# Kernel optimization log

Hardware: AMD Instinct MI355X
Metric: run time of the kernel (lower is better)

Reference implementation:

```python
import jax, jax.numpy as jnp
import numpy as np

# LLaMA-style decoder config (shrunken for reference): L layers, hidden D, H heads,
# SwiGLU width F, vocab V, LoRA rank R.
B, S, D, H, F, V, L, R = 2, 512, 1024, 16, 4096, 32000, 2, 16
DH = D // H
LORA_ALPHA = 32.0
EPS = 1e-5
ROPE_THETA = 10000.0


def setup_inputs() -> dict:
    key = jax.random.key(0)
    ks = iter(jax.random.split(key, 40))
    def n(shape, std=0.02):
        return jax.random.normal(next(ks), shape, jnp.float32) * std
    return {
        "input_ids": jax.random.randint(next(ks), (B, S), 0, V),
        "attention_mask": jnp.ones((B, S), jnp.int32),
        "embed": n((V, D)),
        "ln1": jnp.ones((L, D), jnp.float32),
        "ln2": jnp.ones((L, D), jnp.float32),
        "wq": n((L, D, D)), "aq": n((L, D, R)), "bq": n((L, R, D), 0.01),
        "wk": n((L, D, D)), "ak": n((L, D, R)), "bk": n((L, R, D), 0.01),
        "wv": n((L, D, D)), "av": n((L, D, R)), "bv": n((L, R, D), 0.01),
        "wo": n((L, D, D)), "ao": n((L, D, R)), "bo": n((L, R, D), 0.01),
        "wg": n((L, D, F)), "ag": n((L, D, R)), "bg": n((L, R, F), 0.01),
        "wu": n((L, D, F)), "au": n((L, D, R)), "bu": n((L, R, F), 0.01),
        "wd": n((L, F, D)), "ad": n((L, F, R)), "bd": n((L, R, D), 0.01),
        "final_ln": jnp.ones((D,), jnp.float32),
        "lm_head_w": n((D, V)),
        "value_w": n((D, 1)),
        "value_b": jnp.zeros((1,), jnp.float32),
    }


def _rmsnorm(x, w):
    return x * jax.lax.rsqrt(jnp.mean(x * x, axis=-1, keepdims=True) + EPS) * w


def _lin_lora(x, w, a, b):
    # base matmul + low-rank LoRA update scaled by alpha/r (dropout=eval/off)
    return x @ w + ((x @ a) @ b) * (LORA_ALPHA / R)


def _rope_cache(seq_len):
    half = DH // 2
    inv = 1.0 / (ROPE_THETA ** (jnp.arange(half, dtype=jnp.float32) / half))
    ang = jnp.arange(seq_len, dtype=jnp.float32)[:, None] * inv  # [S, half]
    ang = jnp.concatenate([ang, ang], axis=-1)                   # [S, DH]
    return jnp.cos(ang), jnp.sin(ang)


def _apply_rope(x, cos, sin):  # x: [B,S,H,DH]
    h = DH // 2
    rot = jnp.concatenate([-x[..., h:], x[..., :h]], axis=-1)
    return x * cos[None, :, None, :] + rot * sin[None, :, None, :]


def reference(input_ids, attention_mask, embed, ln1, ln2,
              wq, aq, bq, wk, ak, bk, wv, av, bv, wo, ao, bo,
              wg, ag, bg, wu, au, bu, wd, ad, bd,
              final_ln, lm_head_w, value_w, value_b):
    h = embed[input_ids]  # [B,S,D]
    cos, sin = _rope_cache(S)
    causal = jnp.tril(jnp.ones((S, S), bool))
    keep = causal[None, None, :, :] & (attention_mask[:, None, None, :] > 0)
    bias = jnp.where(keep, 0.0, -1e9)  # [B,1,S,S]
    scale = 1.0 / jnp.sqrt(jnp.float32(DH))

    for i in range(L):
        # --- self-attention block ---
        x = _rmsnorm(h, ln1[i])
        q = _lin_lora(x, wq[i], aq[i], bq[i]).reshape(B, S, H, DH)
        k = _lin_lora(x, wk[i], ak[i], bk[i]).reshape(B, S, H, DH)
        v = _lin_lora(x, wv[i], av[i], bv[i]).reshape(B, S, H, DH)
        q = _apply_rope(q, cos, sin)
        k = _apply_rope(k, cos, sin)
        scores = jnp.einsum("bqhd,bkhd->bhqk", q, k) * scale + bias
        attn = jax.nn.softmax(scores, axis=-1)
        o = jnp.einsum("bhqk,bkhd->bqhd", attn, v).reshape(B, S, D)
        h = h + _lin_lora(o, wo[i], ao[i], bo[i])
        # --- SwiGLU MLP block ---
        x = _rmsnorm(h, ln2[i])
        g = jax.nn.silu(_lin_lora(x, wg[i], ag[i], bg[i]))
        u = _lin_lora(x, wu[i], au[i], bu[i])
        h = h + _lin_lora(g * u, wd[i], ad[i], bd[i])

    h = _rmsnorm(h, final_ln)          # HF hidden_states[-1] is post final norm
    logits = h @ lm_head_w             # [B,S,V]
    values = (h @ value_w)[..., 0] + value_b[0]  # [B,S] (squeeze(-1))
    return logits, values
```

## Files before the change

### kernel.cpp

```cpp
#include <hip/hip_runtime.h>
#include <math.h>

constexpr int B = 2, S = 512, D = 1024, H = 16, F = 4096, V = 32000, L = 2, R = 16, DH = 64;
constexpr int BS = B * S;
constexpr float LORA_SCALE = 2.0f;
constexpr float EPS = 1e-5f;
constexpr int RS_QKV = 3 * D;
constexpr int RS_GU  = 2 * F;

typedef __attribute__((ext_vector_type(8))) __bf16 bf16x8;
typedef __attribute__((ext_vector_type(4))) float f32x4;

__device__ __forceinline__ unsigned short f2bf(float f) {
  unsigned u = __builtin_bit_cast(unsigned, f);
  unsigned r = (u + 0x7FFFu + ((u >> 16) & 1u)) >> 16;
  return (unsigned short)r;
}
__device__ __forceinline__ float bf2f(unsigned short us) {
  return __builtin_bit_cast(float, (unsigned)us << 16);
}
__device__ __forceinline__ void load_lds16(const void* g, void* l) {
  __builtin_amdgcn_global_load_lds((const __attribute__((address_space(1))) void*)g,
                                   (__attribute__((address_space(3))) void*)l, 16, 0, 0);
}

struct Ptr3 { const float* p[3]; };

__global__ void rope_cache_kernel(float* __restrict__ cosb, float* __restrict__ sinb) {
  int s = blockIdx.x, j = threadIdx.x;
  float inv = __expf(-(float)j * (9.210340371976184f / 32.0f));
  float ang = (float)s * inv;
  float c = cosf(ang), sn = sinf(ang);
  cosb[s * DH + j] = c;  cosb[s * DH + j + 32] = c;
  sinb[s * DH + j] = sn; sinb[s * DH + j + 32] = sn;
}

__global__ void embed_kernel(const int* __restrict__ ids, const float* __restrict__ emb,
                             float* __restrict__ h) {
  int row = blockIdx.x, t = threadIdx.x;
  int id = ids[row];
  ((float4*)(h + (size_t)row * D))[t] = ((const float4*)(emb + (size_t)id * D))[t];
}

__global__ void rmsnorm_bf16_kernel(const float* __restrict__ x, const float* __restrict__ w,
                                    unsigned short* __restrict__ y) {
  int row = blockIdx.x, t = threadIdx.x;
  float4 xv = ((const float4*)(x + (size_t)row * D))[t];
  float ss = xv.x * xv.x + xv.y * xv.y + xv.z * xv.z + xv.w * xv.w;
  __shared__ float red[256];
  red[t] = ss; __syncthreads();
  for (int s2 = 128; s2; s2 >>= 1) { if (t < s2) red[t] += red[t + s2]; __syncthreads(); }
  float rinv = rsqrtf(red[0] * (1.0f / D) + EPS);
  float4 wv = ((const float4*)w)[t];
  ushort4 o;
  o.x = f2bf(xv.x * rinv * wv.x); o.y = f2bf(xv.y * rinv * wv.y);
  o.z = f2bf(xv.z * rinv * wv.z); o.w = f2bf(xv.w * rinv * wv.w);
  ((ushort4*)(y + (size_t)row * D))[t] = o;
}

template <int NA>
__global__ void rms_lora_kernel(const float* __restrict__ hp, const float* __restrict__ w,
                                Ptr3 ap, unsigned short* __restrict__ xbf,
                                unsigned short* __restrict__ t2e) {
  int row = blockIdx.x, t = threadIdx.x;
  int lane = t & 63;
  __shared__ float xs[D];
  __shared__ float red[256];
  float4 xv = ((const float4*)(hp + (size_t)row * D))[t];
  float ss = xv.x * xv.x + xv.y * xv.y + xv.z * xv.z + xv.w * xv.w;
  red[t] = ss; __syncthreads();
  for (int s2 = 128; s2; s2 >>= 1) { if (t < s2) red[t] += red[t + s2]; __syncthreads(); }
  float rinv = rsqrtf(red[0] * (1.0f / D) + EPS);
  float4 wv = ((const float4*)w)[t];
  float4 nx;
  nx.x = xv.x * rinv * wv.x; nx.y = xv.y * rinv * wv.y;
  nx.z = xv.z * rinv * wv.z; nx.w = xv.w * rinv * wv.w;
  xs[t * 4 + 0] = nx.x; xs[t * 4 + 1] = nx.y; xs[t * 4 + 2] = nx.z; xs[t * 4 + 3] = nx.w;
  ushort4 o;
  o.x = f2bf(nx.x); o.y = f2bf(nx.y); o.z = f2bf(nx.z); o.w = f2bf(nx.w);
  ((ushort4*)(xbf + (size_t)row * D))[t] = o;
  if (t >= NA * 16 && t < 64) t2e[(size_t)row * 64 + t] = 0;
  __syncthreads();
  int n = t & 15, g = t >> 4;
#pragma unroll
  for (int ad = 0; ad < NA; ++ad) {
    const float* a = ap.p[ad];
    float s = 0.0f;
    for (int k = g; k < D; k += 16) s = fmaf(xs[k], a[k * 16 + n], s);
    s += __shfl_xor(s, 16);
    s += __shfl_xor(s, 32);
    if (lane < 16) red[(t >> 6) * 16 + n] = s;
    __syncthreads();
    if (t < 16) t2e[(size_t)row * 64 + ad * 16 + t] =
        f2bf(LORA_SCALE * (red[t] + red[t + 16] + red[t + 32] + red[t + 48]));
    if (ad + 1 < NA) __syncthreads();
  }
}

__global__ void lora_o_kernel(const unsigned short* __restrict__ xb, const float* __restrict__ a,
                              unsigned short* __restrict__ t2e) {
  int row = blockIdx.x, t = threadIdx.x;
  int lane = t & 63;
  __shared__ float xs[D];
  __shared__ float red[64];
  for (int k = t; k < D; k += 256) xs[k] = bf2f(xb[(size_t)row * D + k]);
  if (t >= 16 && t < 64) t2e[(size_t)row * 64 + t] = 0;
  __syncthreads();
  int n = t & 15, g = t >> 4;
  float s = 0.0f;
  for (int k = g; k < D; k += 16) s = fmaf(xs[k], a[k * 16 + n], s);
  s += __shfl_xor(s, 16);
  s += __shfl_xor(s, 32);
  if (lane < 16) red[(t >> 6) * 16 + n] = s;
  __syncthreads();
  if (t < 16) t2e[(size_t)row * 64 + t] =
      f2bf(LORA_SCALE * (red[t] + red[t + 16] + red[t + 32] + red[t + 48]));
}

__global__ void silu_lora_kernel(const unsigned short* __restrict__ gub, const float* __restrict__ a,
                                 unsigned short* __restrict__ gbf, unsigned short* __restrict__ t2e) {
  int row = blockIdx.x, t = threadIdx.x;
  int lane = t & 63;
  __shared__ float xs[F];
  __shared__ float red[64];
#pragma unroll
  for (int i2 = 0; i2 < 2; ++i2) {
    int idx = i2 * 256 + t;
    uint4 gv = ((const uint4*)(gub + (size_t)row * RS_GU))[idx];
    uint4 uv = ((const uint4*)(gub + (size_t)row * RS_GU + F))[idx];
    const unsigned* gw = (const unsigned*)&gv;
    const unsigned* uw = (const unsigned*)&uv;
    unsigned short go[8];
#pragma unroll
    for (int q = 0; q < 4; ++q) {
      float g0 = bf2f((unsigned short)(gw[q] & 0xffff)), g1 = bf2f((unsigned short)(gw[q] >> 16));
      float u0 = bf2f((unsigned short)(uw[q] & 0xffff)), u1 = bf2f((unsigned short)(uw[q] >> 16));
      float r0 = g0 / (1.0f + __expf(-g0)) * u0;
      float r1 = g1 / (1.0f + __expf(-g1)) * u1;
      xs[idx * 8 + q * 2] = r0; xs[idx * 8 + q * 2 + 1] = r1;
      go[q * 2] = f2bf(r0); go[q * 2 + 1] = f2bf(r1);
    }
    *(uint4*)(gbf + (size_t)row * F + idx * 8) = *(const uint4*)go;
  }
  if (t >= 16 && t < 64) t2e[(size_t)row * 64 + t] = 0;
  __syncthreads();
  int n = t & 15, g = t >> 4;
  float s = 0.0f;
  for (int k = g; k < F; k += 16) s = fmaf(xs[k], a[k * 16 + n], s);
  s += __shfl_xor(s, 16);
  s += __shfl_xor(s, 32);
  if (lane < 16) red[(t >> 6) * 16 + n] = s;
  __syncthreads();
  if (t < 16) t2e[(size_t)row * 64 + t] =
      f2bf(LORA_SCALE * (red[t] + red[t + 16] + red[t + 32] + red[t + 48]));
}

struct BD { const float* p0; const float* p1; const float* p2;
            unsigned short* dst; int NA; int logW; int nelem; };
struct BDs { BD d[8]; };
__global__ void bext_many_kernel(BDs da) {
  int gid = blockIdx.x * 256 + threadIdx.x;
  int di = 0;
  while (gid >= da.d[di].nelem) { gid -= da.d[di].nelem; ++di; }
  const BD dd = da.d[di];
  int n = gid >> 6, kk = gid & 63;
  int W = 1 << dd.logW;
  int sel = n >> dd.logW;
  const float* bp = (sel == 0) ? dd.p0 : (sel == 1) ? dd.p1 : dd.p2;
  float v = 0.0f;
  if ((kk >> 4) == sel && sel < dd.NA)
    v = bp[(size_t)(kk & 15) * W + (n & (W - 1))];
  dd.dst[(size_t)n * 64 + kk] = f2bf(v);
}

struct TD { const float* src; unsigned short* dst; int K; int N; int nblk; };
struct TDs { TD d[15]; };
__global__ __launch_bounds__(256) void transpose_many_kernel(TDs da) {
  __shared__ unsigned short tile[64 * 136];
  int bid = blockIdx.x;
  int di = 0;
  while (bid >= da.d[di].nblk) { bid -= da.d[di].nblk; ++di; }
  const TD dd = da.d[di];
  int nbx = dd.N >> 6;
  int n0 = (bid % nbx) * 64, k0 = (bid / nbx) * 128;
  int t = threadIdx.x;
  int rr = t >> 4, c4 = (t & 15) << 2;
  float4 v[8];
#pragma unroll
  for (int i = 0; i < 8; ++i)
    v[i] = *(const float4*)(dd.src + (size_t)(k0 + i * 16 + rr) * dd.N + n0 + c4);
#pragma unroll
  for (int i = 0; i < 8; ++i) {
    int row = i * 16 + rr;
    tile[(c4 + 0) * 136 + (row ^ ((((c4 + 0) >> 2) & 7) << 2))] = f2bf(v[i].x);
    tile[(c4 + 1) * 136 + (row ^ ((((c4 + 1) >> 2) & 7) << 2))] = f2bf(v[i].y);
    tile[(c4 + 2) * 136 + (row ^ ((((c4 + 2) >> 2) & 7) << 2))] = f2bf(v[i].z);
    tile[(c4 + 3) * 136 + (row ^ ((((c4 + 3) >> 2) & 7) << 2))] = f2bf(v[i].w);
  }
  __syncthreads();
  ushort4 o[8];
#pragma unroll
  for (int i = 0; i < 8; ++i) {
    int flat = i * 256 + t;
    int n = flat >> 5, cw = flat & 31;
    int kb = (cw * 4) ^ (((n >> 2) & 7) << 2);
    o[i] = *(const ushort4*)(tile + n * 136 + kb);
  }
#pragma unroll
  for (int i = 0; i < 8; ++i) {
    int flat = i * 256 + t;
    int n = flat >> 5, cw = flat & 31;
    *(ushort4*)(dd.dst + (size_t)(n0 + n) * dd.K + k0 + cw * 4) = o[i];
  }
}

template <int BN, bool ACC, bool EXT, int OM>
__global__ __launch_bounds__(256) void gemm_bf16_kernel(
    const unsigned short* __restrict__ A, const unsigned short* __restrict__ Bt,
    void* __restrict__ Cp, int M, int N, int K,
    const unsigned short* __restrict__ Ae, const unsigned short* __restrict__ Be,
    const float* __restrict__ cosb, const float* __restrict__ sinb) {
  constexpr int WM = (BN == 128) ? 2 : 4;
  constexpr int RW = 128 / WM;
  constexpr int MI = RW / 16;
  constexpr int BCH = BN / 32;
  __shared__ __align__(16) unsigned short As[2][128 * 64];
  __shared__ __align__(16) unsigned short Bs[2][BN * 64];
  int t = threadIdx.x;
  int lane = t & 63, wave = t >> 6;
  int wr = (BN == 128) ? (wave >> 1) : wave;
  int wc = (BN == 128) ? (wave & 1) : 0;
  int MT = gridDim.y, NT = gridDim.x;
  int nwg = MT * NT;
  int orig = blockIdx.y * NT + blockIdx.x;
  int qq = nwg >> 3, rr8 = nwg & 7;
  int xcd = orig & 7, pos = orig >> 3;
  int wg = (xcd < rr8) ? (xcd * (qq + 1) + pos) : (rr8 * (qq + 1) + (xcd - rr8) * qq + pos);
  int m0 = (wg % MT) * 128, n0 = (wg / MT) * BN;
  int fr = lane & 15, fq = lane >> 4;
  int xorv = fr & 7;
  f32x4 acc[MI][4] = {};
  int kIters = K / 64;
  int nIters = EXT ? kIters + 1 : kIters;

  auto STAGE = [&](int it, int buf) {
    bool ext = EXT && (it == kIters);
    int k0 = it * 64;
#pragma unroll
    for (int c = 0; c < 4; ++c) {
      int i = c * 256 + t;
      int row = i >> 3, c8 = i & 7;
      int sc = (c8 ^ (row & 7)) * 8;
      const unsigned short* src = ext ? (Ae + (size_t)(m0 + row) * 64 + sc)
                                      : (A + (size_t)(m0 + row) * K + k0 + sc);
      load_lds16(src, &As[buf][i * 8]);
    }
#pragma unroll
    for (int c = 0; c < BCH; ++c) {
      int i = c * 256 + t;
      int row = i >> 3, c8 = i & 7;
      int sc = (c8 ^ (row & 7)) * 8;
      const unsigned short* src = ext ? (Be + (size_t)(n0 + row) * 64 + sc)
                                      : (Bt + (size_t)(n0 + row) * K + k0 + sc);
      load_lds16(src, &Bs[buf][i * 8]);
    }
  };

  STAGE(0, 0);
  if (nIters > 1) STAGE(1, 1);
  int cur = 0;
  for (int it = 0; it < nIters; ++it) {
    if (it + 1 < nIters) {
      if constexpr (BN == 128) asm volatile("s_waitcnt vmcnt(8)" ::: "memory");
      else                     asm volatile("s_waitcnt vmcnt(6)" ::: "memory");
    } else {
      asm volatile("s_waitcnt vmcnt(0)" ::: "memory");
    }
    __builtin_amdgcn_s_barrier();
#pragma unroll
    for (int kk = 0; kk < 2; ++kk) {
      bf16x8 af[MI], bfr[4];
#pragma unroll
      for (int mi = 0; mi < MI; ++mi)
        af[mi] = *(const bf16x8*)(&As[cur][(wr * RW + mi * 16 + fr) * 64 + (((kk * 4 + fq) ^ xorv) << 3)]);
#pragma unroll
      for (int ni = 0; ni < 4; ++ni)
        bfr[ni] = *(const bf16x8*)(&Bs[cur][(wc * 64 + ni * 16 + fr) * 64 + (((kk * 4 + fq) ^ xorv) << 3)]);
#pragma unroll
      for (int mi = 0; mi < MI; ++mi)
#pragma unroll
        for (int ni = 0; ni < 4; ++ni)
          acc[mi][ni] = __builtin_amdgcn_mfma_f32_16x16x32_bf16(af[mi], bfr[ni], acc[mi][ni], 0, 0, 0);
    }
    __builtin_amdgcn_s_barrier();
    if (it + 2 < nIters) STAGE(it + 2, cur);
    cur ^= 1;
  }
  if constexpr (OM == 0) {
    float* C = (float*)Cp;
#pragma unroll
    for (int mi = 0; mi < MI; ++mi)
#pragma unroll
      for (int ni = 0; ni < 4; ++ni)
#pragma unroll
        for (int j = 0; j < 4; ++j) {
          int r = m0 + wr * RW + mi * 16 + fq * 4 + j;
          int cl = n0 + wc * 64 + ni * 16 + fr;
          size_t idx = (size_t)r * N + cl;
          float v = acc[mi][ni][j];
          C[idx] = ACC ? C[idx] + v : v;
        }
  } else {
    unsigned short* Cb = (unsigned short*)Cp;
#pragma unroll
    for (int mi = 0; mi < MI; ++mi)
#pragma unroll
      for (int j = 0; j < 4; ++j) {
        int r = m0 + wr * RW + mi * 16 + fq * 4 + j;
        if constexpr (OM == 2) {
          int s = r & (S - 1);
#pragma unroll
          for (int ni = 0; ni < 2; ++ni) {
            int cl0 = n0 + wc * 64 + ni * 16 + fr;
            int cl1 = cl0 + 32;
            float x0 = acc[mi][ni][j], x1 = acc[mi][ni + 2][j];
            if (cl0 < 2 * D) {
              int dh = cl0 & 63;
              float cz = cosb[s * DH + dh], sz = sinb[s * DH + dh];
              float y0 = x0 * cz - x1 * sz;
              float y1 = x1 * cz + x0 * sz;
              x0 = y0; x1 = y1;
            }
            Cb[(size_t)r * N + cl0] = f2bf(x0);
            Cb[(size_t)r * N + cl1] = f2bf(x1);
          }
        } else {
#pragma unroll
          for (int ni = 0; ni < 4; ++ni) {
            int cl = n0 + wc * 64 + ni * 16 + fr;
            Cb[(size_t)r * N + cl] = f2bf(acc[mi][ni][j]);
          }
        }
      }
  }
}

__global__ __launch_bounds__(512) void gemm256_kernel(
    const unsigned short* __restrict__ A, const unsigned short* __restrict__ Bt,
    float* __restrict__ C, int M, int N, int K) {
  __shared__ __align__(16) unsigned short As[2][256 * 64];
  __shared__ __align__(16) unsigned short Bs[2][256 * 64];
  int t = threadIdx.x;
  int lane = t & 63, wave = t >> 6;
  int wr = wave >> 2, wc = wave & 3;
  int MT = gridDim.y, NT = gridDim.x;
  int nwg = MT * NT;
  int orig = blockIdx.y * NT + blockIdx.x;
  int qq = nwg >> 3, rr8 = nwg & 7;
  int xcd = orig & 7, pos = orig >> 3;
  int wg = (xcd < rr8) ? (xcd * (qq + 1) + pos) : (rr8 * (qq + 1) + (xcd - rr8) * qq + pos);
  int m0 = (wg % MT) * 256, n0 = (wg / MT) * 256;
  int fr = lane & 15, fq = lane >> 4;
  int xorv = fr & 7;
  f32x4 acc[8][4] = {};
  int kIters = K / 64;

  auto STAGE = [&](int it, int buf) {
    int k0 = it * 64;
#pragma unroll
    for (int c = 0; c < 4; ++c) {
      int i = c * 512 + t;
      int row = i >> 3, c8 = i & 7;
      int sc = (c8 ^ (row & 7)) * 8;
      load_lds16(A + (size_t)(m0 + row) * K + k0 + sc, &As[buf][i * 8]);
    }
#pragma unroll
    for (int c = 0; c < 4; ++c) {
      int i = c * 512 + t;
      int row = i >> 3, c8 = i & 7;
      int sc = (c8 ^ (row & 7)) * 8;
      load_lds16(Bt + (size_t)(n0 + row) * K + k0 + sc, &Bs[buf][i * 8]);
    }
  };

  STAGE(0, 0);
  if (kIters > 1) STAGE(1, 1);
  int cur = 0;
  for (int it = 0; it < kIters; ++it) {
    if (it + 1 < kIters) asm volatile("s_waitcnt vmcnt(8)" ::: "memory");
    else                 asm volatile("s_waitcnt vmcnt(0)" ::: "memory");
    __builtin_amdgcn_s_barrier();
#pragma unroll
    for (int kk = 0; kk < 2; ++kk) {
      bf16x8 af[8], bfr[4];
#pragma unroll
      for (int mi = 0; mi < 8; ++mi)
        af[mi] = *(const bf16x8*)(&As[cur][(wr * 128 + mi * 16 + fr) * 64 + (((kk * 4 + fq) ^ xorv) << 3)]);
#pragma unroll
      for (int ni = 0; ni < 4; ++ni)
        bfr[ni] = *(const bf16x8*)(&Bs[cur][(wc * 64 + ni * 16 + fr) * 64 + (((kk * 4 + fq) ^ xorv) << 3)]);
#pragma unroll
      for (int mi = 0; mi < 8; ++mi)
#pragma unroll
        for (int ni = 0; ni < 4; ++ni)
          acc[mi][ni] = __builtin_amdgcn_mfma_f32_16x16x32_bf16(af[mi], bfr[ni], acc[mi][ni], 0, 0, 0);
    }
    __builtin_amdgcn_s_barrier();
    if (it + 2 < kIters) STAGE(it + 2, cur);
    cur ^= 1;
  }
#pragma unroll
  for (int mi = 0; mi < 8; ++mi)
#pragma unroll
    for (int ni = 0; ni < 4; ++ni)
#pragma unroll
      for (int j = 0; j < 4; ++j) {
        int r = m0 + wr * 128 + mi * 16 + fq * 4 + j;
        int cl = n0 + wc * 64 + ni * 16 + fr;
        C[(size_t)r * N + cl] = acc[mi][ni][j];
      }
}

__global__ __launch_bounds__(256) void attn_mfma_kernel(
    const unsigned short* __restrict__ qkvb, const int* __restrict__ amask,
    unsigned short* __restrict__ o) {
  __shared__ unsigned short Qs[64 * 72];
  __shared__ unsigned short Ks[64 * 72];
  __shared__ unsigned short Vt[64 * 72];
  __shared__ unsigned short Ps[4][16 * 72];
  __shared__ float msk[64];
  int bid = blockIdx.x;
  int qt = bid & 7, hh = (bid >> 3) & (H - 1), b = bid >> 7;
  int t = threadIdx.x;
  int lane = t & 63, w = t >> 6;
  int fr = lane & 15, fq = lane >> 4;
  size_t rowbase = (size_t)b * S;
  int q0 = qt * 64;
  const float scale = 0.125f;
#pragma unroll
  for (int c = 0; c < 2; ++c) {
    int i = c * 256 + t;
    int row = i >> 3, ch = i & 7;
    *(uint4*)(Qs + row * 72 + ch * 8) =
        *(const uint4*)(qkvb + (rowbase + q0 + row) * RS_QKV + hh * DH + ch * 8);
  }
  f32x4 oacc[4] = {};
  float m_old[4] = {-1e30f, -1e30f, -1e30f, -1e30f};
  float l[4] = {};
  int qbase = q0 + w * 16;
  for (int kt = 0; kt <= qt; ++kt) {
    int kk0 = kt * 64;
#pragma unroll
    for (int c = 0; c < 2; ++c) {
      int i = c * 256 + t;
      int row = i >> 3, ch = i & 7;
      uint4 kv = *(const uint4*)(qkvb + (rowbase + kk0 + row) * RS_QKV + D + hh * DH + ch * 8);
      *(uint4*)(Ks + row * 72 + ch * 8) = kv;
    }
#pragma unroll
    for (int c = 0; c < 2; ++c) {
      int idx = c * 256 + t;
      int rp = idx >> 4, dg = idx & 15;
      const unsigned short* vsrc = qkvb + (rowbase + kk0 + rp * 2) * RS_QKV + 2 * D + hh * DH + dg * 4;
      uint2 lo = *(const uint2*)vsrc;
      uint2 hi = *(const uint2*)(vsrc + RS_QKV);
      const unsigned short* ls = (const unsigned short*)&lo;
      const unsigned short* hs = (const unsigned short*)&hi;
#pragma unroll
      for (int q = 0; q < 4; ++q) {
        unsigned pk = (unsigned)ls[q] | ((unsigned)hs[q] << 16);
        *(unsigned*)(Vt + (dg * 4 + q) * 72 + rp * 2) = pk;
      }
    }
    if (t < 64) msk[t] = (amask[b * S + kk0 + t] > 0) ? 0.0f : -1e9f;
    __syncthreads();
    bf16x8 aq[2];
    aq[0] = *(const bf16x8*)(Qs + (w * 16 + fr) * 72 + fq * 8);
    aq[1] = *(const bf16x8*)(Qs + (w * 16 + fr) * 72 + 32 + fq * 8);
    f32x4 sacc[4];
#pragma unroll
    for (int ct = 0; ct < 4; ++ct) {
      bf16x8 bk0 = *(const bf16x8*)(Ks + (ct * 16 + fr) * 72 + fq * 8);
      bf16x8 bk1 = *(const bf16x8*)(Ks + (ct * 16 + fr) * 72 + 32 + fq * 8);
      f32x4 z = {};
      z = __builtin_amdgcn_mfma_f32_16x16x32_bf16(aq[0], bk0, z, 0, 0, 0);
      sacc[ct] = __builtin_amdgcn_mfma_f32_16x16x32_bf16(aq[1], bk1, z, 0, 0, 0);
    }
    float sv[4][4];
#pragma unroll
    for (int ct = 0; ct < 4; ++ct) {
      int kg = kk0 + ct * 16 + fr;
      float mk = msk[ct * 16 + fr];
#pragma unroll
      for (int j = 0; j < 4; ++j) {
        int qg = qbase + fq * 4 + j;
        float s = sacc[ct][j] * scale + mk;
        sv[ct][j] = (kg > qg) ? -1e9f : s;
      }
    }
    float mnew[4], f[4], rsum[4];
#pragma unroll
    for (int j = 0; j < 4; ++j) {
      float mt = fmaxf(fmaxf(sv[0][j], sv[1][j]), fmaxf(sv[2][j], sv[3][j]));
      for (int off = 1; off < 16; off <<= 1) mt = fmaxf(mt, __shfl_xor(mt, off));
      mnew[j] = fmaxf(m_old[j], mt);
      f[j] = __expf(m_old[j] - mnew[j]);
      float rs = 0.0f;
#pragma unroll
      for (int ct = 0; ct < 4; ++ct) {
        float e = __expf(sv[ct][j] - mnew[j]);
        sv[ct][j] = e;
        rs += e;
      }
      for (int off = 1; off < 16; off <<= 1) rs += __shfl_xor(rs, off);
      rsum[j] = rs;
      l[j] = l[j] * f[j] + rsum[j];
      m_old[j] = mnew[j];
#pragma unroll
      for (int dt = 0; dt < 4; ++dt) oacc[dt][j] *= f[j];
    }
#pragma unroll
    for (int ct = 0; ct < 4; ++ct)
#pragma unroll
      for (int j = 0; j < 4; ++j)
        Ps[w][(fq * 4 + j) * 72 + ct * 16 + fr] = f2bf(sv[ct][j]);
    __syncthreads();
    bf16x8 pa[2];
    pa[0] = *(const bf16x8*)(&Ps[w][fr * 72 + fq * 8]);
    pa[1] = *(const bf16x8*)(&Ps[w][fr * 72 + 32 + fq * 8]);
#pragma unroll
    for (int dt = 0; dt < 4; ++dt) {
      bf16x8 vb0 = *(const bf16x8*)(Vt + (dt * 16 + fr) * 72 + fq * 8);
      bf16x8 vb1 = *(const bf16x8*)(Vt + (dt * 16 + fr) * 72 + 32 + fq * 8);
      oacc[dt] = __builtin_amdgcn_mfma_f32_16x16x32_bf16(pa[0], vb0, oacc[dt], 0, 0, 0);
      oacc[dt] = __builtin_amdgcn_mfma_f32_16x16x32_bf16(pa[1], vb1, oacc[dt], 0, 0, 0);
    }
    __syncthreads();
  }
#pragma unroll
  for (int j = 0; j < 4; ++j) {
    float rinv = 1.0f / l[j];
    int qrow = qbase + fq * 4 + j;
#pragma unroll
    for (int dt = 0; dt < 4; ++dt)
      o[(rowbase + qrow) * D + hh * DH + dt * 16 + fr] = f2bf(oacc[dt][j] * rinv);
  }
}

__global__ void value_kernel(const unsigned short* __restrict__ hf, const float* __restrict__ vw,
                             const float* __restrict__ vb, float* __restrict__ out) {
  int row = blockIdx.x, t = threadIdx.x;
  float acc = 0.0f;
  for (int d = t; d < D; d += 256) acc = fmaf(bf2f(hf[(size_t)row * D + d]), vw[d], acc);
  __shared__ float red[256];
  red[t] = acc; __syncthreads();
  for (int s2 = 128; s2; s2 >>= 1) { if (t < s2) red[t] += red[t + s2]; __syncthreads(); }
  if (t == 0) out[row] = red[0] + vb[0];
}

extern "C" void kernel_launch(void* const* d_in, const int* in_sizes, int n_in,
                              void* d_out, int out_size, void* d_ws, size_t ws_size,
                              hipStream_t stream) {
  const int*   ids     = (const int*)d_in[0];
  const int*   amask   = (const int*)d_in[1];
  const float* emb     = (const float*)d_in[2];
  const float* ln1     = (const float*)d_in[3];
  const float* ln2     = (const float*)d_in[4];
  const float* wq = (const float*)d_in[5],  *aq = (const float*)d_in[6],  *bq = (const float*)d_in[7];
  const float* wk = (const float*)d_in[8],  *ak = (const float*)d_in[9],  *bk = (const float*)d_in[10];
  const float* wv = (const float*)d_in[11], *av = (const float*)d_in[12], *bv = (const float*)d_in[13];
  const float* wo = (const float*)d_in[14], *ao = (const float*)d_in[15], *bo = (const float*)d_in[16];
  const float* wg = (const float*)d_in[17], *ag = (const float*)d_in[18], *bg = (const float*)d_in[19];
  const float* wu = (const float*)d_in[20], *au = (const float*)d_in[21], *bu = (const float*)d_in[22];
  const float* wd = (const float*)d_in[23], *ad = (const float*)d_in[24], *bd = (const float*)d_in[25];
  const float* final_ln  = (const float*)d_in[26];
  const float* lm_head_w = (const float*)d_in[27];
  const float* value_w   = (const float*)d_in[28];
  const float* value_b   = (const float*)d_in[29];

  float* out    = (float*)d_out;
  float* logits = out;
  float* values = out + (size_t)BS * V;

  float* Wf = (float*)d_ws;
  float* cosb = Wf; Wf += S * DH;
  float* sinb = Wf; Wf += S * DH;
  float* h    = Wf; Wf += (size_t)BS * D;
  unsigned short* Wb = (unsigned short*)Wf;
  unsigned short* x_bf  = Wb; Wb += (size_t)BS * D;
  unsigned short* t2e   = Wb; Wb += (size_t)BS * 64;
  unsigned short* qg    = Wb; Wb += (size_t)BS * F;
  unsigned short* gu_bf = Wb; Wb += (size_t)BS * RS_GU;
  unsigned short* wqkvT = Wb; Wb += (size_t)L * 3 * D * D;
  unsigned short* woT   = Wb; Wb += (size_t)L * D * D;
  unsigned short* wguT  = Wb; Wb += (size_t)L * 2 * D * F;
  unsigned short* wdT   = Wb; Wb += (size_t)L * F * D;
  unsigned short* lmT   = Wb; Wb += (size_t)D * V;
  unsigned short* beQKV = Wb; Wb += (size_t)L * 3 * D * 64;
  unsigned short* beO   = Wb; Wb += (size_t)L * D * 64;
  unsigned short* beGU  = Wb; Wb += (size_t)L * 2 * F * 64;
  unsigned short* beD   = Wb; Wb += (size_t)L * D * 64;
  unsigned short* qkv_bf = qg;
  unsigned short* gbf    = qg;
  unsigned short* obf    = gu_bf;

  TDs td; int tblocks = 0; int di = 0;
  auto addT = [&](const float* s, unsigned short* dp, int K_, int N_) {
    td.d[di] = {s, dp, K_, N_, (K_ / 128) * (N_ / 64)};
    tblocks += td.d[di].nblk; ++di;
  };
  for (int l = 0; l < L; ++l) {
    size_t DD = (size_t)D * D, DF = (size_t)D * F;
    addT(wq + l * DD, wqkvT + (size_t)l * 3 * DD, D, D);
    addT(wk + l * DD, wqkvT + (size_t)l * 3 * DD + DD, D, D);
    addT(wv + l * DD, wqkvT + (size_t)l * 3 * DD + 2 * DD, D, D);
    addT(wo + l * DD, woT + l * DD, D, D);
    addT(wg + l * DF, wguT + (size_t)l * 2 * DF, D, F);
    addT(wu + l * DF, wguT + (size_t)l * 2 * DF + DF, D, F);
    addT(wd + l * DF, wdT + l * DF, F, D);
  }
  addT(lm_head_w, lmT, D, V);
  transpose_many_kernel<<<dim3(tblocks), 256, 0, stream>>>(td);

  BDs bd2; int belems = 0; di = 0;
  auto addB = [&](const float* p0, const float* p1, const float* p2,
                  unsigned short* dst, int NA, int logW, int N_) {
    bd2.d[di] = {p0, p1, p2, dst, NA, logW, N_ * 64};
    belems += N_ * 64; ++di;
  };
  for (int l = 0; l < L; ++l) {
    size_t oRD = (size_t)l * R * D, oRF = (size_t)l * R * F;
    addB(bq + oRD, bk + oRD, bv + oRD, beQKV + (size_t)l * 3 * D * 64, 3, 10, 3 * D);
    addB(bo + oRD, nullptr, nullptr,   beO   + (size_t)l * D * 64,     1, 10, D);
    addB(bg + oRF, bu + oRF, nullptr,  beGU  + (size_t)l * 2 * F * 64, 2, 12, 2 * F);
    addB(bd + oRD, nullptr, nullptr,   beD   + (size_t)l * D * 64,     1, 10, D);
  }
  bext_many_kernel<<<dim3(belems / 256), 256, 0, stream>>>(bd2);

  rope_cache_kernel<<<dim3(S), dim3(32), 0, stream>>>(cosb, sinb);
  embed_kernel<<<dim3(BS), dim3(256), 0, stream>>>(ids, emb, h);

  for (int l = 0; l < L; ++l) {
    size_t DD = (size_t)D * D, DF = (size_t)D * F;
    size_t oDR = (size_t)l * D * R, oFR = (size_t)l * F * R;

    { Ptr3 ap = {{aq + oDR, ak + oDR, av + oDR}};
      rms_lora_kernel<3><<<dim3(BS), 256, 0, stream>>>(h, ln1 + (size_t)l * D, ap, x_bf, t2e); }
    gemm_bf16_kernel<128, false, true, 2><<<dim3(3 * D / 128, BS / 128), 256, 0, stream>>>(
        x_bf, wqkvT + (size_t)l * 3 * DD, qkv_bf, BS, 3 * D, D,
        t2e, beQKV + (size_t)l * 3 * D * 64, cosb, sinb);

    attn_mfma_kernel<<<dim3(B * H * (S / 64)), 256, 0, stream>>>(qkv_bf, amask, obf);

    lora_o_kernel<<<dim3(BS), 256, 0, stream>>>(obf, ao + oDR, t2e);
    gemm_bf16_kernel<64, true, true, 0><<<dim3(D / 64, BS / 128), 256, 0, stream>>>(
        obf, woT + l * DD, h, BS, D, D, t2e, beO + (size_t)l * D * 64, nullptr, nullptr);

    { Ptr3 ap = {{ag + oDR, au + oDR, nullptr}};
      rms_lora_kernel<2><<<dim3(BS), 256, 0, stream>>>(h, ln2 + (size_t)l * D, ap, x_bf, t2e); }
    gemm_bf16_kernel<128, false, true, 1><<<dim3(2 * F / 128, BS / 128), 256, 0, stream>>>(
        x_bf, wguT + (size_t)l * 2 * DF, gu_bf, BS, 2 * F, D,
        t2e, beGU + (size_t)l * 2 * F * 64, nullptr, nullptr);

    silu_lora_kernel<<<dim3(BS), 256, 0, stream>>>(gu_bf, ad + oFR, gbf, t2e);

    gemm_bf16_kernel<64, true, true, 0><<<dim3(D / 64, BS / 128), 256, 0, stream>>>(
        gbf, wdT + l * DF, h, BS, D, F, t2e, beD + (size_t)l * D * 64, nullptr, nullptr);
  }

  rmsnorm_bf16_kernel<<<dim3(BS), 256, 0, stream>>>(h, final_ln, x_bf);
  gemm256_kernel<<<dim3(V / 256, BS / 256), 512, 0, stream>>>(x_bf, lmT, logits, BS, V, D);
  value_kernel<<<dim3(BS), 256, 0, stream>>>(x_bf, value_w, value_b, values);
}
```

Measured before the change: 1.004 ms.

## Widen weight transpose tiles, fuse value head into final norm, raise MFMA priority

The weight transpose kernel now handles 256-row K tiles with a new XOR swizzle and writes 16-byte vectors, which halves the block count and widens the stores. The value-head dot product is folded into the final RMSNorm kernel and uses fp32 normalized values, which removes one launch and a re-read of the bf16 activations. The bf16 GEMM main loop raises wave priority around the MFMA section. Risks are higher register and LDS use in the transpose kernel and a slight numeric change in the value output.

```diff
diff --git a/kernel.cpp b/kernel.cpp
--- a/kernel.cpp
+++ b/kernel.cpp
@@ -42,8 +42,9 @@
   ((float4*)(h + (size_t)row * D))[t] = ((const float4*)(emb + (size_t)id * D))[t];
 }
 
-__global__ void rmsnorm_bf16_kernel(const float* __restrict__ x, const float* __restrict__ w,
-                                    unsigned short* __restrict__ y) {
+__global__ void rmsnorm_value_kernel(const float* __restrict__ x, const float* __restrict__ w,
+                                     const float* __restrict__ vw, const float* __restrict__ vb,
+                                     unsigned short* __restrict__ y, float* __restrict__ values) {
   int row = blockIdx.x, t = threadIdx.x;
   float4 xv = ((const float4*)(x + (size_t)row * D))[t];
   float ss = xv.x * xv.x + xv.y * xv.y + xv.z * xv.z + xv.w * xv.w;
@@ -52,10 +53,18 @@
   for (int s2 = 128; s2; s2 >>= 1) { if (t < s2) red[t] += red[t + s2]; __syncthreads(); }
   float rinv = rsqrtf(red[0] * (1.0f / D) + EPS);
   float4 wv = ((const float4*)w)[t];
+  float4 nx;
+  nx.x = xv.x * rinv * wv.x; nx.y = xv.y * rinv * wv.y;
+  nx.z = xv.z * rinv * wv.z; nx.w = xv.w * rinv * wv.w;
   ushort4 o;
-  o.x = f2bf(xv.x * rinv * wv.x); o.y = f2bf(xv.y * rinv * wv.y);
-  o.z = f2bf(xv.z * rinv * wv.z); o.w = f2bf(xv.w * rinv * wv.w);
+  o.x = f2bf(nx.x); o.y = f2bf(nx.y); o.z = f2bf(nx.z); o.w = f2bf(nx.w);
   ((ushort4*)(y + (size_t)row * D))[t] = o;
+  float4 vv = ((const float4*)vw)[t];
+  float vd = nx.x * vv.x + nx.y * vv.y + nx.z * vv.z + nx.w * vv.w;
+  __syncthreads();
+  red[t] = vd; __syncthreads();
+  for (int s2 = 128; s2; s2 >>= 1) { if (t < s2) red[t] += red[t + s2]; __syncthreads(); }
+  if (t == 0) values[row] = red[0] + vb[0];
 }
 
 template <int NA>
@@ -176,41 +185,37 @@
 struct TD { const float* src; unsigned short* dst; int K; int N; int nblk; };
 struct TDs { TD d[15]; };
 __global__ __launch_bounds__(256) void transpose_many_kernel(TDs da) {
-  __shared__ unsigned short tile[64 * 136];
+  __shared__ unsigned short tile[64 * 264];
   int bid = blockIdx.x;
   int di = 0;
   while (bid >= da.d[di].nblk) { bid -= da.d[di].nblk; ++di; }
   const TD dd = da.d[di];
   int nbx = dd.N >> 6;
-  int n0 = (bid % nbx) * 64, k0 = (bid / nbx) * 128;
+  int n0 = (bid % nbx) * 64, k0 = (bid / nbx) * 256;
   int t = threadIdx.x;
   int rr = t >> 4, c4 = (t & 15) << 2;
-  float4 v[8];
-#pragma unroll
-  for (int i = 0; i < 8; ++i)
+  float4 v[16];
+#pragma unroll
+  for (int i = 0; i < 16; ++i)
     v[i] = *(const float4*)(dd.src + (size_t)(k0 + i * 16 + rr) * dd.N + n0 + c4);
 #pragma unroll
-  for (int i = 0; i < 8; ++i) {
-    int row = i * 16 + rr;
-    tile[(c4 + 0) * 136 + (row ^ ((((c4 + 0) >> 2) & 7) << 2))] = f2bf(v[i].x);
-    tile[(c4 + 1) * 136 + (row ^ ((((c4 + 1) >> 2) & 7) << 2))] = f2bf(v[i].y);
-    tile[(c4 + 2) * 136 + (row ^ ((((c4 + 2) >> 2) & 7) << 2))] = f2bf(v[i].z);
-    tile[(c4 + 3) * 136 + (row ^ ((((c4 + 3) >> 2) & 7) << 2))] = f2bf(v[i].w);
+  for (int i = 0; i < 16; ++i) {
+    int k = i * 16 + rr;
+#pragma unroll
+    for (int j = 0; j < 4; ++j) {
+      int n = c4 + j;
+      float e = (j == 0) ? v[i].x : (j == 1) ? v[i].y : (j == 2) ? v[i].z : v[i].w;
+      tile[n * 264 + (k ^ ((n & 3) << 3))] = f2bf(e);
+    }
   }
   __syncthreads();
-  ushort4 o[8];
 #pragma unroll
   for (int i = 0; i < 8; ++i) {
     int flat = i * 256 + t;
     int n = flat >> 5, cw = flat & 31;
-    int kb = (cw * 4) ^ (((n >> 2) & 7) << 2);
-    o[i] = *(const ushort4*)(tile + n * 136 + kb);
-  }
-#pragma unroll
-  for (int i = 0; i < 8; ++i) {
-    int flat = i * 256 + t;
-    int n = flat >> 5, cw = flat & 31;
-    *(ushort4*)(dd.dst + (size_t)(n0 + n) * dd.K + k0 + cw * 4) = o[i];
+    int kb = (cw * 8) ^ ((n & 3) << 3);
+    *(uint4*)(dd.dst + (size_t)(n0 + n) * dd.K + k0 + cw * 8) =
+        *(const uint4*)(tile + n * 264 + kb);
   }
 }
 
@@ -390,6 +395,7 @@
     if (it + 1 < kIters) asm volatile("s_waitcnt vmcnt(8)" ::: "memory");
     else                 asm volatile("s_waitcnt vmcnt(0)" ::: "memory");
     __builtin_amdgcn_s_barrier();
+    __builtin_amdgcn_s_setprio(1);
 #pragma unroll
     for (int kk = 0; kk < 2; ++kk) {
       bf16x8 af[8], bfr[4];
@@ -405,6 +411,7 @@
         for (int ni = 0; ni < 4; ++ni)
           acc[mi][ni] = __builtin_amdgcn_mfma_f32_16x16x32_bf16(af[mi], bfr[ni], acc[mi][ni], 0, 0, 0);
     }
+    __builtin_amdgcn_s_setprio(0);
     __builtin_amdgcn_s_barrier();
     if (it + 2 < kIters) STAGE(it + 2, cur);
     cur ^= 1;
@@ -545,17 +552,6 @@
     for (int dt = 0; dt < 4; ++dt)
       o[(rowbase + qrow) * D + hh * DH + dt * 16 + fr] = f2bf(oacc[dt][j] * rinv);
   }
-}
-
-__global__ void value_kernel(const unsigned short* __restrict__ hf, const float* __restrict__ vw,
-                             const float* __restrict__ vb, float* __restrict__ out) {
-  int row = blockIdx.x, t = threadIdx.x;
-  float acc = 0.0f;
-  for (int d = t; d < D; d += 256) acc = fmaf(bf2f(hf[(size_t)row * D + d]), vw[d], acc);
-  __shared__ float red[256];
-  red[t] = acc; __syncthreads();
-  for (int s2 = 128; s2; s2 >>= 1) { if (t < s2) red[t] += red[t + s2]; __syncthreads(); }
-  if (t == 0) out[row] = red[0] + vb[0];
 }
 
 extern "C" void kernel_launch(void* const* d_in, const int* in_sizes, int n_in,
@@ -606,7 +602,7 @@
 
   TDs td; int tblocks = 0; int di = 0;
   auto addT = [&](const float* s, unsigned short* dp, int K_, int N_) {
-    td.d[di] = {s, dp, K_, N_, (K_ / 128) * (N_ / 64)};
+    td.d[di] = {s, dp, K_, N_, (K_ / 256) * (N_ / 64)};
     tblocks += td.d[di].nblk; ++di;
   };
   for (int l = 0; l < L; ++l) {
@@ -668,7 +664,6 @@
         gbf, wdT + l * DF, h, BS, D, F, t2e, beD + (size_t)l * D * 64, nullptr, nullptr);
   }
 
-  rmsnorm_bf16_kernel<<<dim3(BS), 256, 0, stream>>>(h, final_ln, x_bf);
+  rmsnorm_value_kernel<<<dim3(BS), 256, 0, stream>>>(h, final_ln, value_w, value_b, x_bf, values);
   gemm256_kernel<<<dim3(V / 256, BS / 256), 512, 0, stream>>>(x_bf, lmT, logits, BS, V, D);
-  value_kernel<<<dim3(BS), 256, 0, stream>>>(x_bf, value_w, value_b, values);
-}
+}
```

Result: no change. 1.006 ms (+0.1%).
